# Kernel tuning notes

Hardware: AMD Instinct MI355X
Metric: run time of the kernel (lower is better)

Reference implementation:

```python
import jax, jax.numpy as jnp
import numpy as np

N_NODES = 8192
D_FEAT = 128
R_BITS = 8      # rows per band
B_BANDS = 64    # number of LSH bands
D_THRESH = 0.25 # cosine-distance threshold from LSH(z, d=0.25, ...)


def setup_inputs() -> dict:
    key = jax.random.key(0)
    k1, k2, k3 = jax.random.split(key, 3)
    z = jax.random.normal(k1, (N_NODES, D_FEAT), dtype=jnp.float32)
    # random hyperplanes for signed-projection LSH: r*b = 512 planes
    H = jax.random.normal(k2, (D_FEAT, R_BITS * B_BANDS), dtype=jnp.float32)
    edge_index = jax.random.randint(k3, (2, N_NODES * 16), 0, N_NODES, dtype=jnp.int64)
    return {"z": z, "H": H, "edge_index": edge_index}


def reference(z, H, edge_index):
    # edge_index is unused by forward_all (kept for signature fidelity).
    N = z.shape[0]
    # --- hyperplane LSH signatures ---
    bits = (z @ H) > 0                              # [N, r*b] bool
    bits = bits.reshape(N, B_BANDS, R_BITS)         # [N, b, r]
    powers = (2 ** jnp.arange(R_BITS)).astype(jnp.int32)
    codes = jnp.sum(bits.astype(jnp.int32) * powers, axis=-1)  # [N, b] band hash codes

    # --- candidate pairs: collide in at least one band (OR over bands) ---
    def band_or(mask, c):  # c: [N] codes for one band
        return mask | (c[:, None] == c[None, :]), None
    collide, _ = jax.lax.scan(band_or, jnp.zeros((N, N), dtype=bool), codes.T)

    # --- exact cosine similarity on candidates ---
    zn = z / jnp.linalg.norm(z, axis=1, keepdims=True)
    S = zn @ zn.T                                   # [N, N] cosine similarity
    dist = 1.0 - S                                  # cosine distance

    eye = jnp.eye(N, dtype=bool)
    # pairs kept by LSH: colliding, within distance threshold, off-diagonal
    keep = collide & (dist < D_THRESH) & (~eye)
    # adjacency[v1, v2] = 1 - dist = cos_sim (sigmoid=True path); identity on diagonal
    A = jnp.where(keep, S, 0.0) + eye.astype(S.dtype)
    return A
```

## Files before the change

### kernel.cpp

```cpp
#include <hip/hip_runtime.h>
#include <hip/hip_bf16.h>

#define N_NODES 8192
#define D_FEAT 128

#define ZN_BYTES (2u * 1024u * 1024u)
#define LIST_CAP 1024

typedef __bf16 bf16x8 __attribute__((ext_vector_type(8)));
typedef float f32x4 __attribute__((ext_vector_type(4)));

__device__ __forceinline__ void vm0_barrier() {
  asm volatile("s_waitcnt vmcnt(0) lgkmcnt(0)\n\ts_barrier" ::: "memory");
}

__device__ __forceinline__ void async_copy16(void* lds, const void* g) {
  __builtin_amdgcn_global_load_lds(
      (const __attribute__((address_space(1))) void*)g,
      (__attribute__((address_space(3))) void*)lds, 16, 0, 0);
}

__device__ __attribute__((noinline)) bool lsh_collide(
    const float* __restrict__ z, const float* __restrict__ H, int i, int j) {
  for (int b = 0; b < 64; ++b) {
    unsigned ci = 0, cj = 0;
    for (int bit = 0; bit < 8; ++bit) {
      int col = b * 8 + bit;
      float di = 0.f, dj = 0.f;
      for (int k = 0; k < D_FEAT; ++k) {
        float h = H[(size_t)k * 512 + col];
        di += z[(size_t)i * D_FEAT + k] * h;
        dj += z[(size_t)j * D_FEAT + k] * h;
      }
      if (di > 0.f) ci |= (1u << bit);
      if (dj > 0.f) cj |= (1u << bit);
    }
    if (ci == cj) return true;
  }
  return false;
}

__device__ __forceinline__ unsigned pack_bf16x2(float x, float y) {
  __hip_bfloat16 bx = __float2bfloat16(x), by = __float2bfloat16(y);
  return (unsigned)(*(unsigned short*)&bx) |
         ((unsigned)(*(unsigned short*)&by) << 16);
}

__global__ __launch_bounds__(256) void eye_kernel(f32x4* __restrict__ out) {
  unsigned base = (unsigned)blockIdx.x * 8192u + (unsigned)threadIdx.x;
#pragma unroll
  for (int k = 0; k < 32; ++k) {
    unsigned c = base + (unsigned)k * 256u;
    unsigned row = c >> 11;
    unsigned col0 = (c & 2047u) << 2;
    f32x4 v;
    v[0] = (col0 == row) ? 1.0f : 0.0f;
    v[1] = (col0 + 1u == row) ? 1.0f : 0.0f;
    v[2] = (col0 + 2u == row) ? 1.0f : 0.0f;
    v[3] = (col0 + 3u == row) ? 1.0f : 0.0f;
    out[c] = v;
  }
}

__global__ __launch_bounds__(256) void norm_kernel(const float* __restrict__ z,
                                                   uint4* __restrict__ zn,
                                                   int* __restrict__ cnt) {
  if (blockIdx.x == 0 && threadIdx.x == 0) *cnt = 0;
  int gt = (int)blockIdx.x * 256 + (int)threadIdx.x;
  int row = gt >> 3, oct = gt & 7;
  const float4* src = (const float4*)(z + (size_t)row * D_FEAT + oct * 16);
  float4 v[4];
#pragma unroll
  for (int c = 0; c < 4; ++c) v[c] = src[c];
  float ss = 0.f;
#pragma unroll
  for (int c = 0; c < 4; ++c)
    ss += v[c].x * v[c].x + v[c].y * v[c].y + v[c].z * v[c].z + v[c].w * v[c].w;
  ss += __shfl_xor(ss, 1);
  ss += __shfl_xor(ss, 2);
  ss += __shfl_xor(ss, 4);
  float inv = rsqrtf(ss);
  int blk = row >> 7, r = row & 127;
  uint4* dst = zn + (size_t)blk * 2048 + r * 16;
#pragma unroll
  for (int c2 = 0; c2 < 2; ++c2) {
    float4 a = v[2 * c2], b = v[2 * c2 + 1];
    uint4 o;
    o.x = pack_bf16x2(a.x * inv, a.y * inv);
    o.y = pack_bf16x2(a.z * inv, a.w * inv);
    o.z = pack_bf16x2(b.x * inv, b.y * inv);
    o.w = pack_bf16x2(b.z * inv, b.w * inv);
    dst[(oct * 2 + c2) ^ (r & 15)] = o;
  }
}

__global__ __launch_bounds__(256, 2) void sim_kernel(const uint4* __restrict__ zn,
                                                     int* __restrict__ cnt,
                                                     int4* __restrict__ list) {
  __shared__ __align__(16) unsigned char smem[65536];

  int tid = threadIdx.x;
  int b = (int)blockIdx.x;
  int bm0 = b & 7;
  int bn = b >> 3;

  int wv = tid >> 6, lane = tid & 63;
  int wm = (wv >> 1) * 64, wn = (wv & 1) * 64;
  int m16 = lane & 15, g = lane >> 4;

  {
    const uint4* gB = zn + (size_t)bn * 2048;
    const uint4* gA = zn + (size_t)(bm0 * 8) * 2048;
#pragma unroll
    for (int i = 0; i < 8; ++i) {
      int c = i * 256 + tid;
      async_copy16(smem + 32768 + c * 16, gB + c);
      async_copy16(smem + c * 16, gA + c);
    }
  }
  vm0_barrier();

  bf16x8 fbr[16];
  {
    unsigned short (*Bs)[128] = (unsigned short (*)[128])(smem + 32768);
#pragma unroll
    for (int kc = 0; kc < 4; ++kc) {
      int cs = ((kc * 4 + g) ^ m16) * 8;
#pragma unroll
      for (int tt = 0; tt < 4; ++tt)
        fbr[kc * 4 + tt] = *(const bf16x8*)&Bs[wn + tt * 16 + m16][cs];
    }
  }

  for (int t = 0; t < 8; ++t) {
    int bm = bm0 * 8 + t;
    unsigned char* cur = smem + (t & 1) * 32768;
    unsigned char* nxt = smem + ((t + 1) & 1) * 32768;

    vm0_barrier();

    if (t < 7) {
      const uint4* gA = zn + (size_t)(bm + 1) * 2048;
#pragma unroll
      for (int i = 0; i < 8; ++i) {
        int c = i * 256 + tid;
        async_copy16(nxt + c * 16, gA + c);
      }
    }

    unsigned short (*As)[128] = (unsigned short (*)[128])cur;
    f32x4 acc[4][4] = {};
#pragma unroll
    for (int kc = 0; kc < 4; ++kc) {
      bf16x8 fa[4];
      int cs = ((kc * 4 + g) ^ m16) * 8;
#pragma unroll
      for (int tt = 0; tt < 4; ++tt)
        fa[tt] = *(const bf16x8*)&As[wm + tt * 16 + m16][cs];
#pragma unroll
      for (int tm = 0; tm < 4; ++tm)
#pragma unroll
        for (int tn = 0; tn < 4; ++tn)
          acc[tm][tn] = __builtin_amdgcn_mfma_f32_16x16x32_bf16(fa[tm], fbr[kc * 4 + tn], acc[tm][tn], 0, 0, 0);
    }

#pragma unroll
    for (int tm = 0; tm < 4; ++tm)
#pragma unroll
      for (int tn = 0; tn < 4; ++tn) {
        f32x4 c = acc[tm][tn];
        float m4 = fmaxf(fmaxf(c[0], c[1]), fmaxf(c[2], c[3]));
        if (m4 > 0.75f) {
          int j = bn * 128 + wn + tn * 16 + m16;
#pragma unroll
          for (int r = 0; r < 4; ++r) {
            int i = bm * 128 + wm + tm * 16 + g * 4 + r;
            if (i != j && c[r] > 0.75f) {
              int idx = atomicAdd(cnt, 1);
              if (idx < LIST_CAP)
                list[idx] = make_int4(i, j, __float_as_int(c[r]), 0);
            }
          }
        }
      }
  }
}

__global__ __launch_bounds__(256) void fixup_kernel(const float* __restrict__ z,
                                                    const float* __restrict__ H,
                                                    const int* __restrict__ cnt,
                                                    const int4* __restrict__ list,
                                                    float* __restrict__ out) {
  int n = *cnt;
  if (n > LIST_CAP) n = LIST_CAP;
  for (int e = (int)threadIdx.x; e < n; e += 256) {
    int i = list[e].x, j = list[e].y;
    float s = __int_as_float(list[e].z);
    if (lsh_collide(z, H, i, j)) out[(size_t)i * N_NODES + j] = s;
  }
}

extern "C" void kernel_launch(void* const* d_in, const int* in_sizes, int n_in,
                              void* d_out, int out_size, void* d_ws, size_t ws_size,
                              hipStream_t stream) {
  const float* z = (const float*)d_in[0];
  const float* H = (const float*)d_in[1];
  float* out = (float*)d_out;
  unsigned char* ws = (unsigned char*)d_ws;
  uint4* zn = (uint4*)ws;
  int* cnt = (int*)(ws + ZN_BYTES);
  int4* list = (int4*)(ws + ZN_BYTES + 16);
  (void)ws_size;

  eye_kernel<<<2048, 256, 0, stream>>>((f32x4*)out);
  norm_kernel<<<256, 256, 0, stream>>>(z, zn, cnt);
  sim_kernel<<<512, 256, 0, stream>>>(zn, cnt, list);
  fixup_kernel<<<1, 256, 0, stream>>>(z, H, cnt, list, out);
}
```

Measured before the change: 287.6 us.

## Fuse identity/zero output fill into similarity kernel and relax pipeline wait

Result: faster. 277.9 us (-3.4%).

```diff
diff --git a/kernel.cpp b/kernel.cpp
--- a/kernel.cpp
+++ b/kernel.cpp
@@ -10,6 +10,9 @@
 typedef __bf16 bf16x8 __attribute__((ext_vector_type(8)));
 typedef float f32x4 __attribute__((ext_vector_type(4)));
 
+__device__ __forceinline__ void stage_barrier() {
+  asm volatile("s_waitcnt vmcnt(16) lgkmcnt(0)\n\ts_barrier" ::: "memory");
+}
 __device__ __forceinline__ void vm0_barrier() {
   asm volatile("s_waitcnt vmcnt(0) lgkmcnt(0)\n\ts_barrier" ::: "memory");
 }
@@ -46,22 +49,6 @@
          ((unsigned)(*(unsigned short*)&by) << 16);
 }
 
-__global__ __launch_bounds__(256) void eye_kernel(f32x4* __restrict__ out) {
-  unsigned base = (unsigned)blockIdx.x * 8192u + (unsigned)threadIdx.x;
-#pragma unroll
-  for (int k = 0; k < 32; ++k) {
-    unsigned c = base + (unsigned)k * 256u;
-    unsigned row = c >> 11;
-    unsigned col0 = (c & 2047u) << 2;
-    f32x4 v;
-    v[0] = (col0 == row) ? 1.0f : 0.0f;
-    v[1] = (col0 + 1u == row) ? 1.0f : 0.0f;
-    v[2] = (col0 + 2u == row) ? 1.0f : 0.0f;
-    v[3] = (col0 + 3u == row) ? 1.0f : 0.0f;
-    out[c] = v;
-  }
-}
-
 __global__ __launch_bounds__(256) void norm_kernel(const float* __restrict__ z,
                                                    uint4* __restrict__ zn,
                                                    int* __restrict__ cnt) {
@@ -95,6 +82,7 @@
 }
 
 __global__ __launch_bounds__(256, 2) void sim_kernel(const uint4* __restrict__ zn,
+                                                     float* __restrict__ out,
                                                      int* __restrict__ cnt,
                                                      int4* __restrict__ list) {
   __shared__ __align__(16) unsigned char smem[65536];
@@ -108,6 +96,9 @@
   int wm = (wv >> 1) * 64, wn = (wv & 1) * 64;
   int m16 = lane & 15, g = lane >> 4;
 
+  int srow = tid >> 5;
+  int schunk = tid & 31;
+
   {
     const uint4* gB = zn + (size_t)bn * 2048;
     const uint4* gA = zn + (size_t)(bm0 * 8) * 2048;
@@ -137,7 +128,7 @@
     unsigned char* cur = smem + (t & 1) * 32768;
     unsigned char* nxt = smem + ((t + 1) & 1) * 32768;
 
-    vm0_barrier();
+    stage_barrier();
 
     if (t < 7) {
       const uint4* gA = zn + (size_t)(bm + 1) * 2048;
@@ -145,6 +136,30 @@
       for (int i = 0; i < 8; ++i) {
         int c = i * 256 + tid;
         async_copy16(nxt + c * 16, gA + c);
+      }
+    }
+
+    {
+      float* obase = out + (size_t)(bm * 128) * N_NODES + bn * 128;
+      if (bm == bn) {
+#pragma unroll
+        for (int it = 0; it < 16; ++it) {
+          int r = it * 8 + srow;
+          f32x4 v;
+          int c0 = schunk * 4;
+          v[0] = (r == c0) ? 1.0f : 0.0f;
+          v[1] = (r == c0 + 1) ? 1.0f : 0.0f;
+          v[2] = (r == c0 + 2) ? 1.0f : 0.0f;
+          v[3] = (r == c0 + 3) ? 1.0f : 0.0f;
+          *(f32x4*)&obase[(size_t)r * N_NODES + c0] = v;
+        }
+      } else {
+        f32x4 zv = {0.f, 0.f, 0.f, 0.f};
+#pragma unroll
+        for (int it = 0; it < 16; ++it) {
+          int r = it * 8 + srow;
+          *(f32x4*)&obase[(size_t)r * N_NODES + schunk * 4] = zv;
+        }
       }
     }
 
@@ -212,8 +227,7 @@
   int4* list = (int4*)(ws + ZN_BYTES + 16);
   (void)ws_size;
 
-  eye_kernel<<<2048, 256, 0, stream>>>((f32x4*)out);
   norm_kernel<<<256, 256, 0, stream>>>(z, zn, cnt);
-  sim_kernel<<<512, 256, 0, stream>>>(zn, cnt, list);
+  sim_kernel<<<512, 256, 0, stream>>>(zn, out, cnt, list);
   fixup_kernel<<<1, 256, 0, stream>>>(z, H, cnt, list, out);
 }
```
